# Kernel optimization log

Hardware: AMD Instinct MI355X
Metric: run time of the kernel (lower is better)

The kernel has to match this reference:

```python
import jax, jax.numpy as jnp
import numpy as np

N = 4096       # num nodes
E = 131072     # num edges (avg degree 32)
IN = 256
HID = 512
OUT = 64


def _linear_params(k, fan_in, fan_out):
    kw, kb = jax.random.split(k)
    s = 1.0 / np.sqrt(fan_in)
    W = jax.random.uniform(kw, (fan_in, fan_out), jnp.float32, -s, s)
    b = jax.random.uniform(kb, (fan_out,), jnp.float32, -s, s)
    return W, b


def setup_inputs() -> dict:
    key = jax.random.key(0)
    ks = jax.random.split(key, 8)
    x = jax.random.normal(ks[0], (N, IN), jnp.float32)
    edge_index = jax.random.randint(ks[1], (2, E), 0, N, jnp.int32)
    ego_W, ego_b = _linear_params(ks[2], IN, HID)
    cut_W, cut_b = _linear_params(ks[3], IN, HID)
    glob_W, glob_b = _linear_params(ks[4], IN, HID)
    fc_W, fc_b = _linear_params(ks[5], 3 * HID, OUT)
    return dict(x=x, edge_index=edge_index, ego_W=ego_W, ego_b=ego_b,
                cut_W=cut_W, cut_b=cut_b, glob_W=glob_W, glob_b=glob_b,
                fc_W=fc_W, fc_b=fc_b)


def reference(x, edge_index, ego_W, ego_b, cut_W, cut_b, glob_W, glob_b, fc_W, fc_b):
    src, dst = edge_index[0], edge_index[1]
    n = x.shape[0]

    # --- extract_ego_subgraph: mean of x over the unique 2-hop in-neighborhood
    # (k_hop_subgraph flow='source_to_target': walk edges backward), incl. self.
    # B[t, s] = 1 iff edge s -> t exists.
    B = jnp.zeros((n, n), jnp.float32).at[dst, src].set(1.0)
    eye = jnp.eye(n, dtype=jnp.float32)
    reach = ((eye + B + B @ B) > 0).astype(jnp.float32)   # [N, N] bool-as-float
    ego_feat = (reach @ x) / reach.sum(axis=1, keepdims=True)  # counts >= 1 (self)

    # --- extract_cut_subgraph: drop a random half of the edges, then mean of
    # target features over kept out-edges per source node; fallback to x.
    perm = jax.random.permutation(jax.random.key(42), E)
    keep = jnp.ones(E, bool).at[perm[: E // 2]].set(False).astype(x.dtype)  # [E]
    sums = jax.ops.segment_sum(x[dst] * keep[:, None], src, num_segments=n)
    cnt = jax.ops.segment_sum(keep, src, num_segments=n)
    cut_feat = jnp.where((cnt > 0)[:, None], sums / jnp.maximum(cnt, 1.0)[:, None], x)

    # --- MessagePassingLayer: relu(scatter_add(linear(x)[src] -> dst))
    def mp(feat, W, b):
        h = feat @ W + b
        agg = jax.ops.segment_sum(h[src], dst, num_segments=n)
        return jax.nn.relu(agg)

    ego_enc = mp(ego_feat, ego_W, ego_b)
    cut_enc = mp(cut_feat, cut_W, cut_b)
    glob_enc = x @ glob_W + glob_b

    combined = jnp.concatenate([ego_enc, cut_enc, glob_enc], axis=-1)  # [N, 3H]
    out = combined @ fc_W + fc_b
    return jax.nn.log_softmax(out, axis=1)
```

## Files before the change

kernel.cpp:

```cpp
#include <hip/hip_runtime.h>

#define NN 4096
#define NE 131072
#define DIN 256
#define DHID 512
#define DOUT 64
#define DCAT 1536
#define NBINS 65536
#define HALF_E 65536

typedef __attribute__((ext_vector_type(8))) short short8;
typedef __attribute__((ext_vector_type(4))) float f32x4;

__device__ inline unsigned short bf16rne(float f){
  unsigned u = __float_as_uint(f);
  unsigned r = u + 0x7FFFu + ((u>>16)&1u);
  return (unsigned short)(r>>16);
}
__device__ inline float bf2f(unsigned short u){ return __uint_as_float(((unsigned)u)<<16); }

struct K2 { unsigned a, b; };
__host__ __device__ constexpr unsigned rotl32(unsigned x, unsigned d){ return (x<<d)|(x>>(32u-d)); }
__host__ __device__ constexpr K2 tf2x32(unsigned k0, unsigned k1, unsigned x0, unsigned x1){
  unsigned k2 = k0 ^ k1 ^ 0x1BD11BDAu;
  x0 += k0; x1 += k1;
  x0+=x1; x1=rotl32(x1,13); x1^=x0;
  x0+=x1; x1=rotl32(x1,15); x1^=x0;
  x0+=x1; x1=rotl32(x1,26); x1^=x0;
  x0+=x1; x1=rotl32(x1, 6); x1^=x0;
  x0+=k1; x1+=k2+1u;
  x0+=x1; x1=rotl32(x1,17); x1^=x0;
  x0+=x1; x1=rotl32(x1,29); x1^=x0;
  x0+=x1; x1=rotl32(x1,16); x1^=x0;
  x0+=x1; x1=rotl32(x1,24); x1^=x0;
  x0+=k2; x1+=k0+2u;
  x0+=x1; x1=rotl32(x1,13); x1^=x0;
  x0+=x1; x1=rotl32(x1,15); x1^=x0;
  x0+=x1; x1=rotl32(x1,26); x1^=x0;
  x0+=x1; x1=rotl32(x1, 6); x1^=x0;
  x0+=k0; x1+=k1+3u;
  x0+=x1; x1=rotl32(x1,17); x1^=x0;
  x0+=x1; x1=rotl32(x1,29); x1^=x0;
  x0+=x1; x1=rotl32(x1,16); x1^=x0;
  x0+=x1; x1=rotl32(x1,24); x1^=x0;
  x0+=k1; x1+=k2+4u;
  x0+=x1; x1=rotl32(x1,13); x1^=x0;
  x0+=x1; x1=rotl32(x1,15); x1^=x0;
  x0+=x1; x1=rotl32(x1,26); x1^=x0;
  x0+=x1; x1=rotl32(x1, 6); x1^=x0;
  x0+=k2; x1+=k0+5u;
  return K2{x0,x1};
}
static_assert(tf2x32(0u,0u,0u,2u).a==4146024105u, "threefry mismatch o0");
static_assert(tf2x32(0u,0u,0u,2u).b==2718843009u, "threefry mismatch o1");
static_assert(tf2x32(0u,0u,1u,3u).a==967050713u,  "threefry mismatch o0b");
static_assert(tf2x32(0u,0u,1u,3u).b==1272950319u, "threefry mismatch o1b");

constexpr K2 E0 = tf2x32(0u,42u,0u,0u);
constexpr K2 E1 = tf2x32(0u,42u,0u,1u);
constexpr unsigned SK1A = E1.a, SK1B = E1.b;
constexpr K2 F1 = tf2x32(E0.a,E0.b,0u,1u);
constexpr unsigned SK2A = F1.a, SK2B = F1.b;

#define MED_CAP 64

__device__ inline void tconv(const float* __restrict__ src, unsigned short* __restrict__ dst,
                             int R, int C, int r0, int c0){
  __shared__ unsigned short tile[64][72];
  int t = threadIdx.x;
  int tr = t>>2, tc = (t&3)*16;
  #pragma unroll
  for (int u=0;u<16;u++)
    tile[tr][tc+u] = bf16rne(src[(size_t)(r0+tr)*C + c0 + tc + u]);
  __syncthreads();
  unsigned short v[16];
  #pragma unroll
  for (int u=0;u<16;u++) v[u] = tile[tc+u][tr];
  uint4* vv = (uint4*)v;
  uint4* o = (uint4*)&dst[(size_t)(c0+tr)*R + r0 + tc];
  o[0] = vv[0]; o[1] = vv[1];
}

__global__ void front_k(const int* __restrict__ ei,
                        unsigned* __restrict__ keys1, unsigned* __restrict__ keys2,
                        unsigned* __restrict__ hist1, unsigned* __restrict__ hist2,
                        unsigned* __restrict__ indeg, unsigned* __restrict__ outdeg,
                        unsigned* __restrict__ bits,
                        const float* __restrict__ x, unsigned short* __restrict__ x_bf,
                        unsigned short* __restrict__ xT_bf,
                        const float* __restrict__ W0, unsigned short* __restrict__ WT0,
                        const float* __restrict__ W1, unsigned short* __restrict__ WT1,
                        const float* __restrict__ W2, unsigned short* __restrict__ WT2,
                        const float* __restrict__ fcW, unsigned short* __restrict__ fcWT){
  int b = blockIdx.x, t = threadIdx.x;
  if (b < 512){
    unsigned e = b*256u + t;
    K2 r1 = tf2x32(SK1A, SK1B, 0u, e);
    unsigned k1 = r1.a ^ r1.b;
    K2 r2 = tf2x32(SK2A, SK2B, 0u, e);
    unsigned k2 = r2.a ^ r2.b;
    keys1[e] = k1; keys2[e] = k2;
    atomicAdd(&hist1[k1>>16], 1u);
    atomicAdd(&hist2[k2>>16], 1u);
    unsigned s = (unsigned)ei[e], d = (unsigned)ei[NE+e];
    atomicAdd(&outdeg[s], 1u);
    atomicAdd(&indeg[d], 1u);
    atomicOr(&bits[d*128 + (s>>5)], 1u << (s&31));
    if (e < NN) atomicOr(&bits[e*128 + (e>>5)], 1u << (e&31));
    return;
  }
  int b2 = b - 512;
  if (b2 < 256){
    __shared__ unsigned short tile[64][72];
    int r0 = (b2>>2)*64, c0 = (b2&3)*64;
    int tr = t>>2, tc = (t&3)*16;
    #pragma unroll
    for (int u=0;u<16;u++)
      tile[tr][tc+u] = bf16rne(x[(size_t)(r0+tr)*DIN + c0 + tc + u]);
    __syncthreads();
    unsigned short vr[16];
    #pragma unroll
    for (int u=0;u<16;u++) vr[u] = tile[tr][tc+u];
    uint4* rv = (uint4*)vr;
    uint4* xo = (uint4*)&x_bf[(size_t)(r0+tr)*DIN + c0 + tc];
    xo[0] = rv[0]; xo[1] = rv[1];
    unsigned short v[16];
    #pragma unroll
    for (int u=0;u<16;u++) v[u] = tile[tc+u][tr];
    uint4* vv = (uint4*)v;
    uint4* o = (uint4*)&xT_bf[(size_t)(c0+tr)*NN + r0 + tc];
    o[0] = vv[0]; o[1] = vv[1];
  } else if (b2 < 352){
    int idx = b2 - 256;
    int z = idx >> 5, tl = idx & 31;
    const float* src = z==0?W0 : z==1?W1 : W2;
    unsigned short* dst = z==0?WT0 : z==1?WT1 : WT2;
    tconv(src, dst, DIN, DHID, (tl>>3)*64, (tl&7)*64);
  } else {
    int by = b2 - 352;
    tconv(fcW, fcWT, DCAT, DOUT, by*64, 0);
  }
}

__global__ void scanAll_k(const unsigned* __restrict__ in0, const unsigned* __restrict__ in1,
                          const unsigned* __restrict__ in2, const unsigned* __restrict__ in3,
                          unsigned* __restrict__ o0, unsigned* __restrict__ o1,
                          unsigned* __restrict__ o2, unsigned* __restrict__ o3,
                          unsigned* __restrict__ c0, unsigned* __restrict__ c1,
                          unsigned* __restrict__ c2, unsigned* __restrict__ c3,
                          unsigned* __restrict__ flags, const unsigned* __restrict__ hist2,
                          unsigned* __restrict__ med){
  int y = blockIdx.y;
  int nblk = (y<2) ? (NBINS/256) : (NN/256);
  int xb = blockIdx.x;
  if (xb >= nblk) return;
  const unsigned* in = y==0?in0 : y==1?in1 : y==2?in2 : in3;
  unsigned* o        = y==0?o0  : y==1?o1  : y==2?o2  : o3;
  unsigned* c        = y==0?c0  : y==1?c1  : y==2?c2  : c3;
  __shared__ unsigned s[256];
  __shared__ unsigned base_s;
  int t = threadIdx.x; unsigned i = xb*256u + t;
  unsigned v = in[i]; s[t] = v; __syncthreads();
  for (int off=1; off<256; off<<=1){
    unsigned u = (t>=off)?s[t-off]:0u; __syncthreads();
    s[t]+=u; __syncthreads();
  }
  unsigned excl = s[t]-v;
  unsigned total = s[255];
  unsigned* f = flags + y*256;
  if (xb == 0){
    if (t==0){ atomicExch(&f[0], 0x80000000u | total); base_s = 0u; }
  } else {
    if (t==0) atomicExch(&f[xb], 0x40000000u | total);
    if (t < 64){
      unsigned base = 0; int start = xb-1; int done = 0;
      while (!done && start >= 0){
        int idx = start - t;
        unsigned fv = 0;
        if (idx >= 0){
          do { fv = atomicAdd(&f[idx], 0u); } while (!(fv & 0xC0000000u));
        }
        unsigned long long pm = __ballot(idx >= 0 && (fv & 0x80000000u));
        unsigned contrib;
        if (pm){
          int plane = __ffsll((long long)pm) - 1;
          contrib = (idx >= 0 && t <= plane) ? (fv & 0x3FFFFFFFu) : 0u;
          done = 1;
        } else {
          contrib = (idx >= 0) ? (fv & 0x3FFFFFFFu) : 0u;
          start -= 64;
        }
        for (int oo=32; oo>0; oo>>=1) contrib += __shfl_xor(contrib, oo, 64);
        base += contrib;
      }
      if (t==0){ atomicExch(&f[xb], 0x80000000u | (base + total)); base_s = base; }
    }
  }
  __syncthreads();
  unsigned res = excl + base_s;
  o[i] = res; c[i] = res;
  if (y==1){
    unsigned hv = hist2[i];
    if (res <= HALF_E && HALF_E < res + hv){ med[0] = i; med[1] = res; }
  }
}

__global__ void scat1med_k(const unsigned* __restrict__ keys1, const unsigned* __restrict__ keys2,
                           unsigned* __restrict__ cursor, unsigned* __restrict__ slow,
                           unsigned* __restrict__ stb, unsigned* __restrict__ med){
  int e = blockIdx.x*256 + threadIdx.x;
  unsigned k = keys1[e];
  unsigned p = atomicAdd(&cursor[k>>16], 1u);
  slow[p] = k & 0xFFFFu; stb[p] = (unsigned)e;
  unsigned k2 = keys2[e];
  if ((k2>>16) == med[0]){
    unsigned idx = atomicAdd(&med[2], 1u);
    if (idx < MED_CAP){ med[8+idx] = k2 & 0xFFFFu; med[72+idx] = (unsigned)e; }
  }
}

__global__ void rank1med_k(const unsigned* __restrict__ keys1, const unsigned* __restrict__ prefix,
                           const unsigned* __restrict__ hist, const unsigned* __restrict__ slow,
                           const unsigned* __restrict__ stb, unsigned* __restrict__ rank1,
                           unsigned* __restrict__ med){
  int b = blockIdx.x, t = threadIdx.x;
  if (b == NE/256){
    unsigned n = med[2]; if (n > MED_CAP) n = MED_CAP;
    unsigned qcut = HALF_E - med[1];
    if (t < (int)n){
      unsigned lo = med[8+t], rk = med[72+t], pos = 0;
      for (unsigned j=0;j<n;j++){
        unsigned lj = med[8+j], rj = med[72+j];
        if (lj < lo || (lj==lo && rj < rk)) pos++;
      }
      if (pos == qcut){ med[3] = lo; med[4] = rk; }
    }
    return;
  }
  int e = b*256 + t;
  unsigned k = keys1[e], h = k>>16, lo = k & 0xFFFFu, tb = (unsigned)e;
  unsigned base = prefix[h], n = hist[h], r = 0;
  for (unsigned j=0;j<n;j++){
    unsigned l2 = slow[base+j], t2 = stb[base+j];
    if (l2 < lo || (l2==lo && t2 < tb)) r++;
  }
  rank1[e] = base + r;
}

__global__ void scatter_edges_k(const int* __restrict__ ei, const unsigned* __restrict__ rank1,
                                const unsigned* __restrict__ keys2, const unsigned* __restrict__ med,
                                unsigned* __restrict__ curin, unsigned* __restrict__ curout,
                                unsigned* __restrict__ in_list, unsigned* __restrict__ out_list){
  int e = blockIdx.x*256 + threadIdx.x;
  unsigned s = (unsigned)ei[e], d = (unsigned)ei[NE+e];
  unsigned rk = rank1[e], k2 = keys2[rk];
  unsigned h = k2>>16, lo = k2 & 0xFFFFu;
  unsigned hs = med[0], loc = med[3], rkc = med[4];
  unsigned keep = (h > hs) || (h == hs && (lo > loc || (lo == loc && rk >= rkc)));
  unsigned p = atomicAdd(&curin[d], 1u);  in_list[p] = s;
  unsigned q = atomicAdd(&curout[s], 1u); out_list[q] = d | (keep<<31);
}

__global__ void reachcut_k(const unsigned* __restrict__ bits, const unsigned* __restrict__ in_off,
                           const unsigned* __restrict__ in_list, const unsigned* __restrict__ indeg,
                           unsigned* __restrict__ reach, float* __restrict__ cntinv,
                           const float* __restrict__ x, const unsigned* __restrict__ out_off,
                           const unsigned* __restrict__ outdeg, const unsigned* __restrict__ out_list,
                           unsigned short* __restrict__ cut_bf){
  __shared__ unsigned nbr[256];
  int b = blockIdx.x, t = threadIdx.x;
  if (b < NN){
    __shared__ int ws4[4];
    int i = b;
    unsigned off = in_off[i], deg = indeg[i];
    unsigned acc = (t < 128) ? bits[i*128 + t] : 0u;
    for (unsigned base=0; base<deg; base+=256){
      unsigned ch = min(deg-base, 256u);
      if (t < (int)ch) nbr[t] = in_list[off+base+t];
      __syncthreads();
      if (t < 128){
        #pragma unroll 4
        for (unsigned j=0;j<ch;j++) acc |= bits[nbr[j]*128 + t];
      }
      __syncthreads();
    }
    if (t < 128) reach[i*128 + t] = acc;
    int c = __popc(acc);
    for (int o=32;o>0;o>>=1) c += __shfl_xor(c, o, 64);
    if ((t&63)==0) ws4[t>>6] = c;
    __syncthreads();
    if (t==0) cntinv[i] = 1.0f / (float)(ws4[0]+ws4[1]+ws4[2]+ws4[3]);
  } else {
    int s = b - NN;
    unsigned off = out_off[s], deg = outdeg[s];
    float acc = 0.f; int cnt = 0;
    for (unsigned base=0; base<deg; base+=256){
      unsigned ch = min(deg-base, 256u);
      if (t < (int)ch) nbr[t] = out_list[off+base+t];
      __syncthreads();
      #pragma unroll 4
      for (unsigned j=0;j<ch;j++){
        unsigned v = nbr[j];
        if (v >> 31){ cnt++; acc += x[(size_t)(v & 0xFFFu)*DIN + t]; }
      }
      __syncthreads();
    }
    float v = cnt ? acc / (float)cnt : x[(size_t)s*DIN + t];
    cut_bf[(size_t)s*DIN + t] = bf16rne(v);
  }
}

__global__ void bitgemm_k(const unsigned* __restrict__ reach, const unsigned short* __restrict__ xT,
                          float* __restrict__ pbuf){
  __shared__ __align__(16) unsigned short bt[4][64*32];
  int t = threadIdx.x, w = t>>6, l = t&63;
  int m0 = blockIdx.x*64, n0 = blockIdx.y*64;
  int kbase = blockIdx.z*(NN/4);
  int srow = t>>2, sg = t&3;
  int arow = m0 + 16*w + (l&15);
  int lg = l>>4;
  f32x4 acc[4];
  #pragma unroll
  for (int c=0;c<4;c++) acc[c] = f32x4{0.f,0.f,0.f,0.f};

  for (int it=0; it<8; ++it){
    int kk = kbase + it*128;
    __syncthreads();
    #pragma unroll
    for (int s=0;s<4;s++){
      uint4 v = *(const uint4*)&xT[(size_t)(n0+srow)*NN + kk + 32*s + sg*8];
      *(uint4*)&bt[s][srow*32 + ((sg ^ (srow&3))*8)] = v;
    }
    __syncthreads();
    unsigned rw[4];
    *(uint4*)rw = *(const uint4*)&reach[(size_t)arow*128 + (kk>>5)];
    #pragma unroll
    for (int s=0;s<4;s++){
      unsigned byte = (rw[s] >> (8*lg)) & 0xFFu;
      union { short8 s8; unsigned u[4]; } af;
      #pragma unroll
      for (int pp=0;pp<4;pp++){
        unsigned b0 = (byte>>(2*pp))&1u, b1 = (byte>>(2*pp+1))&1u;
        af.u[pp] = b0*0x3F80u | b1*0x3F800000u;
      }
      #pragma unroll
      for (int c=0;c<4;c++){
        int brow = 16*c + (l&15);
        short8 bf = *(const short8*)&bt[s][brow*32 + ((lg ^ (brow&3))*8)];
        acc[c] = __builtin_amdgcn_mfma_f32_16x16x32_bf16(af.s8, bf, acc[c], 0,0,0);
      }
    }
  }
  size_t zoff = (size_t)blockIdx.z*NN*DIN;
  #pragma unroll
  for (int c=0;c<4;c++){
    #pragma unroll
    for (int r=0;r<4;r++){
      int row = m0 + 16*w + 4*lg + r;
      int col = n0 + 16*c + (l&15);
      pbuf[zoff + (size_t)row*DIN + col] = acc[c][r];
    }
  }
}

__global__ void redscale_k(const float* __restrict__ pbuf, const float* __restrict__ cntinv,
                           unsigned short* __restrict__ ego_bf){
  int g = blockIdx.x*256 + threadIdx.x;
  const size_t S = (size_t)NN*DIN/4;
  const float4* p4 = (const float4*)pbuf;
  float4 a = p4[g], b = p4[g+S], c = p4[g+2*S], d = p4[g+3*S];
  int row = (g*4)>>8;
  float ci = cntinv[row];
  float vx = (a.x+b.x+c.x+d.x)*ci, vy = (a.y+b.y+c.y+d.y)*ci;
  float vz = (a.z+b.z+c.z+d.z)*ci, vw = (a.w+b.w+c.w+d.w)*ci;
  uint2 o;
  o.x = (unsigned)bf16rne(vx) | ((unsigned)bf16rne(vy)<<16);
  o.y = (unsigned)bf16rne(vz) | ((unsigned)bf16rne(vw)<<16);
  ((uint2*)ego_bf)[g] = o;
}

__global__ void aggfeat_k(const unsigned short* __restrict__ ego_bf, const unsigned short* __restrict__ cut_bf,
                          const unsigned* __restrict__ in_off, const unsigned* __restrict__ indeg,
                          const unsigned* __restrict__ in_list,
                          unsigned short* __restrict__ aggE, unsigned short* __restrict__ aggC){
  __shared__ unsigned nbr[256];
  int i = blockIdx.x, t = threadIdx.x;
  unsigned off = in_off[i], deg = indeg[i];
  float ae = 0.f, ac = 0.f;
  for (unsigned base=0; base<deg; base+=256){
    unsigned ch = min(deg-base, 256u);
    if (t < (int)ch) nbr[t] = in_list[off+base+t];
    __syncthreads();
    #pragma unroll 4
    for (unsigned j=0;j<ch;j++){
      unsigned s = nbr[j];
      ae += bf2f(ego_bf[(size_t)s*DIN + t]);
      ac += bf2f(cut_bf[(size_t)s*DIN + t]);
    }
    __syncthreads();
  }
  aggE[(size_t)i*DIN + t] = bf16rne(ae);
  aggC[(size_t)i*DIN + t] = bf16rne(ac);
}

__global__ void gemm3_k(const unsigned short* __restrict__ aggE, const unsigned short* __restrict__ aggC,
                        const unsigned short* __restrict__ xbf,
                        const unsigned short* __restrict__ WTe, const unsigned short* __restrict__ WTc,
                        const unsigned short* __restrict__ WTg,
                        const float* __restrict__ eb, const float* __restrict__ cb, const float* __restrict__ gb,
                        const unsigned* __restrict__ indeg, unsigned short* __restrict__ hcat){
  __shared__ __align__(16) unsigned short at[4][64*32];
  __shared__ __align__(16) unsigned short bt[4][64*32];
  int z = blockIdx.z;
  const unsigned short* A  = z==0? aggE : z==1? aggC : xbf;
  const unsigned short* BT = z==0? WTe  : z==1? WTc  : WTg;
  const float* bias        = z==0? eb   : z==1? cb   : gb;
  int t = threadIdx.x, w = t>>6, l = t&63;
  int n0 = blockIdx.x*64, m0 = blockIdx.y*64;
  int srow = t>>2, sg = t&3;
  int lg = l>>4;
  f32x4 acc[4];
  #pragma unroll
  for (int c=0;c<4;c++) acc[c] = f32x4{0.f,0.f,0.f,0.f};

  for (int it=0; it<2; ++it){
    int kk = it*128;
    __syncthreads();
    #pragma unroll
    for (int s=0;s<4;s++){
      uint4 va = *(const uint4*)&A [(size_t)(m0+srow)*DIN + kk + 32*s + sg*8];
      uint4 vb = *(const uint4*)&BT[(size_t)(n0+srow)*DIN + kk + 32*s + sg*8];
      *(uint4*)&at[s][srow*32 + ((sg ^ (srow&3))*8)] = va;
      *(uint4*)&bt[s][srow*32 + ((sg ^ (srow&3))*8)] = vb;
    }
    __syncthreads();
    int ar = 16*w + (l&15);
    #pragma unroll
    for (int s=0;s<4;s++){
      short8 af = *(const short8*)&at[s][ar*32 + ((lg ^ (ar&3))*8)];
      #pragma unroll
      for (int c=0;c<4;c++){
        int brow = 16*c + (l&15);
        short8 bf = *(const short8*)&bt[s][brow*32 + ((lg ^ (brow&3))*8)];
        acc[c] = __builtin_amdgcn_mfma_f32_16x16x32_bf16(af, bf, acc[c], 0,0,0);
      }
    }
  }
  #pragma unroll
  for (int c=0;c<4;c++){
    #pragma unroll
    for (int r=0;r<4;r++){
      int row = m0 + 16*w + 4*lg + r;
      int col = n0 + 16*c + (l&15);
      float scale = (z<2) ? (float)indeg[row] : 1.0f;
      float v = acc[c][r] + bias[col]*scale;
      if (z<2) v = fmaxf(v, 0.f);
      hcat[(size_t)row*DCAT + z*DHID + col] = bf16rne(v);
    }
  }
}

__global__ void fcsm_k(const unsigned short* __restrict__ hcat, const unsigned short* __restrict__ fcWT,
                       const float* __restrict__ fcb, float* __restrict__ out){
  __shared__ __align__(16) unsigned short at[4][64*32];
  __shared__ __align__(16) unsigned short bt[4][64*32];
  int t = threadIdx.x, w = t>>6, l = t&63;
  int m0 = blockIdx.x*64;
  int srow = t>>2, sg = t&3;
  int lg = l>>4;
  f32x4 acc[4];
  #pragma unroll
  for (int c=0;c<4;c++) acc[c] = f32x4{0.f,0.f,0.f,0.f};

  for (int it=0; it<12; ++it){
    int kk = it*128;
    __syncthreads();
    #pragma unroll
    for (int s=0;s<4;s++){
      uint4 va = *(const uint4*)&hcat [(size_t)(m0+srow)*DCAT + kk + 32*s + sg*8];
      uint4 vb = *(const uint4*)&fcWT[(size_t)srow*DCAT + kk + 32*s + sg*8];
      *(uint4*)&at[s][srow*32 + ((sg ^ (srow&3))*8)] = va;
      *(uint4*)&bt[s][srow*32 + ((sg ^ (srow&3))*8)] = vb;
    }
    __syncthreads();
    int ar = 16*w + (l&15);
    #pragma unroll
    for (int s=0;s<4;s++){
      short8 af = *(const short8*)&at[s][ar*32 + ((lg ^ (ar&3))*8)];
      #pragma unroll
      for (int c=0;c<4;c++){
        int brow = 16*c + (l&15);
        short8 bf = *(const short8*)&bt[s][brow*32 + ((lg ^ (brow&3))*8)];
        acc[c] = __builtin_amdgcn_mfma_f32_16x16x32_bf16(af, bf, acc[c], 0,0,0);
      }
    }
  }
  #pragma unroll
  for (int r=0;r<4;r++){
    int row = m0 + 16*w + 4*lg + r;
    float v0 = acc[0][r] + fcb[(l&15)];
    float v1 = acc[1][r] + fcb[16 + (l&15)];
    float v2 = acc[2][r] + fcb[32 + (l&15)];
    float v3 = acc[3][r] + fcb[48 + (l&15)];
    float m = fmaxf(fmaxf(v0,v1), fmaxf(v2,v3));
    m = fmaxf(m, __shfl_xor(m, 1, 64));
    m = fmaxf(m, __shfl_xor(m, 2, 64));
    m = fmaxf(m, __shfl_xor(m, 4, 64));
    m = fmaxf(m, __shfl_xor(m, 8, 64));
    float s = __expf(v0-m) + __expf(v1-m) + __expf(v2-m) + __expf(v3-m);
    s += __shfl_xor(s, 1, 64);
    s += __shfl_xor(s, 2, 64);
    s += __shfl_xor(s, 4, 64);
    s += __shfl_xor(s, 8, 64);
    float ls = logf(s);
    size_t ro = (size_t)row*DOUT + (l&15);
    out[ro]      = (v0 - m) - ls;
    out[ro + 16] = (v1 - m) - ls;
    out[ro + 32] = (v2 - m) - ls;
    out[ro + 48] = (v3 - m) - ls;
  }
}

static inline size_t alignup(size_t x){ return (x + 255) & ~(size_t)255; }

extern "C" void kernel_launch(void* const* d_in, const int* in_sizes, int n_in,
                              void* d_out, int out_size, void* d_ws, size_t ws_size,
                              hipStream_t stream) {
  const float* x      = (const float*)d_in[0];
  const int*   ei     = (const int*)  d_in[1];
  const float* ego_W  = (const float*)d_in[2];
  const float* ego_b  = (const float*)d_in[3];
  const float* cut_W  = (const float*)d_in[4];
  const float* cut_b  = (const float*)d_in[5];
  const float* glob_W = (const float*)d_in[6];
  const float* glob_b = (const float*)d_in[7];
  const float* fc_W   = (const float*)d_in[8];
  const float* fc_b   = (const float*)d_in[9];
  float* out = (float*)d_out;

  char* base = (char*)d_ws;
  char* p = base;
  #define ALLOC(ty, name, cnt) ty* name = (ty*)p; p += alignup(sizeof(ty)*(size_t)(cnt));
  ALLOC(char,           R0,      (size_t)4*NN*DIN*4);
  ALLOC(unsigned,       bits,    NN*128);
  ALLOC(unsigned,       indeg,   NN);
  ALLOC(unsigned,       outdeg,  NN);
  ALLOC(unsigned,       hist1,   NBINS);
  ALLOC(unsigned,       hist2,   NBINS);
  ALLOC(unsigned,       med,     256);
  ALLOC(unsigned,       flags,   1024);
  char* zero_end = p;
  ALLOC(unsigned,       in_off,  NN);
  ALLOC(unsigned,       out_off, NN);
  ALLOC(unsigned,       curin,   NN);
  ALLOC(unsigned,       curout,  NN);
  ALLOC(unsigned,       in_list, NE);
  ALLOC(unsigned,       out_list,NE);
  ALLOC(unsigned,       reach,   NN*128);
  ALLOC(float,          cntinv,  NN);
  ALLOC(unsigned short, x_bf,    (size_t)NN*DIN);
  ALLOC(unsigned short, xT_bf,   (size_t)DIN*NN);
  ALLOC(unsigned short, ego_bf,  (size_t)NN*DIN);
  ALLOC(unsigned short, cut_bf,  (size_t)NN*DIN);
  ALLOC(unsigned short, aggE_bf, (size_t)NN*DIN);
  ALLOC(unsigned short, aggC_bf, (size_t)NN*DIN);
  ALLOC(unsigned short, egoWT,   (size_t)DHID*DIN);
  ALLOC(unsigned short, cutWT,   (size_t)DHID*DIN);
  ALLOC(unsigned short, globWT,  (size_t)DHID*DIN);
  ALLOC(unsigned short, fcWT,    (size_t)DOUT*DCAT);
  ALLOC(unsigned,       prefix1, NBINS);
  ALLOC(unsigned,       cursor1, NBINS);
  ALLOC(unsigned,       prefix2, NBINS);
  ALLOC(unsigned,       cursor2, NBINS);
  #undef ALLOC
  size_t need = (size_t)(p - base);
  if (ws_size < need){
    hipMemsetAsync(d_out, 0x7F, (size_t)out_size*sizeof(float), stream);
    return;
  }
  float*          pbuf = (float*)R0;
  unsigned short* hcat = (unsigned short*)R0;
  char* q = R0;
  #define OALLOC(ty, name, cnt) ty* name = (ty*)q; q += alignup(sizeof(ty)*(size_t)(cnt));
  OALLOC(unsigned, keys1,  NE);
  OALLOC(unsigned, keys2,  NE);
  OALLOC(unsigned, rank1,  NE);
  OALLOC(unsigned, slow,   NE);
  OALLOC(unsigned, stb,    NE);
  #undef OALLOC

  const int EB = NE/256;

  hipMemsetAsync(bits, 0, (size_t)(zero_end - (char*)bits), stream);
  hipLaunchKernelGGL(front_k, dim3(888), dim3(256), 0, stream,
                     ei, keys1, keys2, hist1, hist2, indeg, outdeg, bits,
                     x, x_bf, xT_bf, ego_W, egoWT, cut_W, cutWT, glob_W, globWT, fc_W, fcWT);
  hipLaunchKernelGGL(scanAll_k, dim3(NBINS/256, 4), dim3(256), 0, stream,
                     hist1, hist2, indeg, outdeg,
                     prefix1, prefix2, in_off, out_off,
                     cursor1, cursor2, curin, curout, flags, hist2, med);
  hipLaunchKernelGGL(scat1med_k, dim3(EB), dim3(256), 0, stream,
                     keys1, keys2, cursor1, slow, stb, med);
  hipLaunchKernelGGL(rank1med_k, dim3(EB+1), dim3(256), 0, stream,
                     keys1, prefix1, hist1, slow, stb, rank1, med);
  hipLaunchKernelGGL(scatter_edges_k, dim3(EB), dim3(256), 0, stream,
                     ei, rank1, keys2, med, curin, curout, in_list, out_list);
  hipLaunchKernelGGL(reachcut_k, dim3(2*NN), dim3(256), 0, stream,
                     bits, in_off, in_list, indeg, reach, cntinv,
                     x, out_off, outdeg, out_list, cut_bf);
  hipLaunchKernelGGL(bitgemm_k, dim3(NN/64, DIN/64, 4), dim3(256), 0, stream, reach, xT_bf, pbuf);
  hipLaunchKernelGGL(redscale_k, dim3((NN*DIN/4)/256), dim3(256), 0, stream, pbuf, cntinv, ego_bf);
  hipLaunchKernelGGL(aggfeat_k, dim3(NN), dim3(256), 0, stream,
                     ego_bf, cut_bf, in_off, indeg, in_list, aggE_bf, aggC_bf);
  hipLaunchKernelGGL(gemm3_k, dim3(DHID/64, NN/64, 3), dim3(256), 0, stream,
                     aggE_bf, aggC_bf, x_bf, egoWT, cutWT, globWT,
                     ego_b, cut_b, glob_b, indeg, hcat);
  hipLaunchKernelGGL(fcsm_k, dim3(NN/64), dim3(256), 0, stream, hcat, fcWT, fc_b, out);
}
```

Before: 181.4 us.

## Fuse rank and edge-scatter kernels, defer keep test to reachcut

The rank kernel and the edge-scatter kernel are merged into one. Each edge's sort rank is packed into the upper bits of its out_list entry. The random-drop keep decision is moved into reachcut_k, which now looks up keys2 by that rank and compares against the median. The low-key and tiebreak arrays are also packed into one 64-bit word, so the rank loop does a single load and a single compare. This removes one launch and the rank1 round trip through memory, but adds a gathered keys2 load per out-edge in reachcut.

```diff
diff --git a/kernel.cpp b/kernel.cpp
--- a/kernel.cpp
+++ b/kernel.cpp
@@ -206,12 +206,12 @@
 }
 
 __global__ void scat1med_k(const unsigned* __restrict__ keys1, const unsigned* __restrict__ keys2,
-                           unsigned* __restrict__ cursor, unsigned* __restrict__ slow,
-                           unsigned* __restrict__ stb, unsigned* __restrict__ med){
+                           unsigned* __restrict__ cursor, unsigned long long* __restrict__ slowstb,
+                           unsigned* __restrict__ med){
   int e = blockIdx.x*256 + threadIdx.x;
   unsigned k = keys1[e];
   unsigned p = atomicAdd(&cursor[k>>16], 1u);
-  slow[p] = k & 0xFFFFu; stb[p] = (unsigned)e;
+  slowstb[p] = ((unsigned long long)(k & 0xFFFFu) << 32) | (unsigned)e;
   unsigned k2 = keys2[e];
   if ((k2>>16) == med[0]){
     unsigned idx = atomicAdd(&med[2], 1u);
@@ -219,9 +219,11 @@
   }
 }
 
-__global__ void rank1med_k(const unsigned* __restrict__ keys1, const unsigned* __restrict__ prefix,
-                           const unsigned* __restrict__ hist, const unsigned* __restrict__ slow,
-                           const unsigned* __restrict__ stb, unsigned* __restrict__ rank1,
+__global__ void rankscat_k(const int* __restrict__ ei, const unsigned* __restrict__ keys1,
+                           const unsigned* __restrict__ prefix, const unsigned* __restrict__ hist,
+                           const unsigned long long* __restrict__ slowstb,
+                           unsigned* __restrict__ curin, unsigned* __restrict__ curout,
+                           unsigned* __restrict__ in_list, unsigned* __restrict__ out_list,
                            unsigned* __restrict__ med){
   int b = blockIdx.x, t = threadIdx.x;
   if (b == NE/256){
@@ -238,27 +240,15 @@
     return;
   }
   int e = b*256 + t;
-  unsigned k = keys1[e], h = k>>16, lo = k & 0xFFFFu, tb = (unsigned)e;
+  unsigned k = keys1[e], h = k>>16;
+  unsigned long long me = ((unsigned long long)(k & 0xFFFFu) << 32) | (unsigned)e;
   unsigned base = prefix[h], n = hist[h], r = 0;
-  for (unsigned j=0;j<n;j++){
-    unsigned l2 = slow[base+j], t2 = stb[base+j];
-    if (l2 < lo || (l2==lo && t2 < tb)) r++;
-  }
-  rank1[e] = base + r;
-}
-
-__global__ void scatter_edges_k(const int* __restrict__ ei, const unsigned* __restrict__ rank1,
-                                const unsigned* __restrict__ keys2, const unsigned* __restrict__ med,
-                                unsigned* __restrict__ curin, unsigned* __restrict__ curout,
-                                unsigned* __restrict__ in_list, unsigned* __restrict__ out_list){
-  int e = blockIdx.x*256 + threadIdx.x;
+  for (unsigned j=0;j<n;j++)
+    r += (slowstb[base+j] < me) ? 1u : 0u;
+  unsigned rk = base + r;
   unsigned s = (unsigned)ei[e], d = (unsigned)ei[NE+e];
-  unsigned rk = rank1[e], k2 = keys2[rk];
-  unsigned h = k2>>16, lo = k2 & 0xFFFFu;
-  unsigned hs = med[0], loc = med[3], rkc = med[4];
-  unsigned keep = (h > hs) || (h == hs && (lo > loc || (lo == loc && rk >= rkc)));
   unsigned p = atomicAdd(&curin[d], 1u);  in_list[p] = s;
-  unsigned q = atomicAdd(&curout[s], 1u); out_list[q] = d | (keep<<31);
+  unsigned q = atomicAdd(&curout[s], 1u); out_list[q] = d | (rk<<12);
 }
 
 __global__ void reachcut_k(const unsigned* __restrict__ bits, const unsigned* __restrict__ in_off,
@@ -266,6 +256,7 @@
                            unsigned* __restrict__ reach, float* __restrict__ cntinv,
                            const float* __restrict__ x, const unsigned* __restrict__ out_off,
                            const unsigned* __restrict__ outdeg, const unsigned* __restrict__ out_list,
+                           const unsigned* __restrict__ keys2, const unsigned* __restrict__ med,
                            unsigned short* __restrict__ cut_bf){
   __shared__ unsigned nbr[256];
   int b = blockIdx.x, t = threadIdx.x;
@@ -291,17 +282,26 @@
     __syncthreads();
     if (t==0) cntinv[i] = 1.0f / (float)(ws4[0]+ws4[1]+ws4[2]+ws4[3]);
   } else {
+    __shared__ unsigned key_s[256];
     int s = b - NN;
     unsigned off = out_off[s], deg = outdeg[s];
+    unsigned hs = med[0], loc = med[3], rkc = med[4];
     float acc = 0.f; int cnt = 0;
     for (unsigned base=0; base<deg; base+=256){
       unsigned ch = min(deg-base, 256u);
-      if (t < (int)ch) nbr[t] = out_list[off+base+t];
+      if (t < (int)ch){
+        unsigned v = out_list[off+base+t];
+        nbr[t] = v;
+        key_s[t] = keys2[v >> 12];
+      }
       __syncthreads();
       #pragma unroll 4
       for (unsigned j=0;j<ch;j++){
-        unsigned v = nbr[j];
-        if (v >> 31){ cnt++; acc += x[(size_t)(v & 0xFFFu)*DIN + t]; }
+        unsigned v = nbr[j], k2 = key_s[j];
+        unsigned rk = v >> 12;
+        unsigned h = k2>>16, lo = k2 & 0xFFFFu;
+        unsigned keep = (h > hs) || (h == hs && (lo > loc || (lo == loc && rk >= rkc)));
+        if (keep){ cnt++; acc += x[(size_t)(v & 0xFFFu)*DIN + t]; }
       }
       __syncthreads();
     }
@@ -582,11 +582,9 @@
   unsigned short* hcat = (unsigned short*)R0;
   char* q = R0;
   #define OALLOC(ty, name, cnt) ty* name = (ty*)q; q += alignup(sizeof(ty)*(size_t)(cnt));
-  OALLOC(unsigned, keys1,  NE);
-  OALLOC(unsigned, keys2,  NE);
-  OALLOC(unsigned, rank1,  NE);
-  OALLOC(unsigned, slow,   NE);
-  OALLOC(unsigned, stb,    NE);
+  OALLOC(unsigned,            keys1,   NE);
+  OALLOC(unsigned,            keys2,   NE);
+  OALLOC(unsigned long long,  slowstb, NE);
   #undef OALLOC
 
   const int EB = NE/256;
@@ -600,14 +598,12 @@
                      prefix1, prefix2, in_off, out_off,
                      cursor1, cursor2, curin, curout, flags, hist2, med);
   hipLaunchKernelGGL(scat1med_k, dim3(EB), dim3(256), 0, stream,
-                     keys1, keys2, cursor1, slow, stb, med);
-  hipLaunchKernelGGL(rank1med_k, dim3(EB+1), dim3(256), 0, stream,
-                     keys1, prefix1, hist1, slow, stb, rank1, med);
-  hipLaunchKernelGGL(scatter_edges_k, dim3(EB), dim3(256), 0, stream,
-                     ei, rank1, keys2, med, curin, curout, in_list, out_list);
+                     keys1, keys2, cursor1, slowstb, med);
+  hipLaunchKernelGGL(rankscat_k, dim3(EB+1), dim3(256), 0, stream,
+                     ei, keys1, prefix1, hist1, slowstb, curin, curout, in_list, out_list, med);
   hipLaunchKernelGGL(reachcut_k, dim3(2*NN), dim3(256), 0, stream,
                      bits, in_off, in_list, indeg, reach, cntinv,
-                     x, out_off, outdeg, out_list, cut_bf);
+                     x, out_off, outdeg, out_list, keys2, med, cut_bf);
   hipLaunchKernelGGL(bitgemm_k, dim3(NN/64, DIN/64, 4), dim3(256), 0, stream, reach, xT_bf, pbuf);
   hipLaunchKernelGGL(redscale_k, dim3((NN*DIN/4)/256), dim3(256), 0, stream, pbuf, cntinv, ego_bf);
   hipLaunchKernelGGL(aggfeat_k, dim3(NN), dim3(256), 0, stream,
```

Measured after the change: 175.2 us. 3.5% less time.
